# Kernel tuning notes

Hardware: AMD Instinct MI355X
Metric: run time of the kernel (lower is better)

## Reference

```python
import jax, jax.numpy as jnp
import numpy as np

BETA = 0.25


def setup_inputs() -> dict:
    key = jax.random.key(0)
    k1, k2 = jax.random.split(key)
    z = jax.random.normal(k1, (16, 2048, 64), dtype=jnp.float32)
    emb = jax.random.uniform(k2, (8192, 64), dtype=jnp.float32)  # uniform_() init
    return {"z": z, "emb": emb}


def reference(z, emb):
    # z: [B, N, D], emb: [K, D]; use_norm=False so norm is identity.
    B, N, D = z.shape
    zf = z.reshape(-1, D)                                   # [B*N, D]
    # Squared euclidean distances; argmin is identical to cdist(p=2) argmin.
    d2 = (
        jnp.sum(zf * zf, axis=1, keepdims=True)
        - 2.0 * (zf @ emb.T)
        + jnp.sum(emb * emb, axis=1)
    )                                                       # [B*N, K]
    idx = jnp.argmin(d2, axis=1)                            # [B*N]
    z_q = emb[idx].reshape(z.shape)                         # [B, N, D]
    loss = BETA * jnp.mean((jax.lax.stop_gradient(z_q) - z) ** 2) + jnp.mean(
        (z_q - jax.lax.stop_gradient(z)) ** 2
    )
    z_q_st = z + jax.lax.stop_gradient(z_q - z)             # straight-through
    return z_q_st, idx, loss
```

## Files before the change

### kernel.cpp

```cpp
#include <hip/hip_runtime.h>
#include <hip/hip_bf16.h>
#include <math.h>

#define D 64
#define K_CODES 8192
#define M_QUERIES 32768
#define SLICES 8
#define CODES_PER_SLICE (K_CODES / SLICES)
#define CHUNK 32
#define NCHUNK (CODES_PER_SLICE / CHUNK)
#define QPB 128
#define TAU_V 4e-3f

typedef __attribute__((ext_vector_type(8))) short bf16x8;
typedef __attribute__((ext_vector_type(4))) float f32x4;
typedef __attribute__((ext_vector_type(16))) float f32x16;

__device__ __forceinline__ unsigned short f2bf(float x) {
    __hip_bfloat16 h = __float2bfloat16(x);
    return *reinterpret_cast<unsigned short*>(&h);
}
__device__ __forceinline__ float bf2f(unsigned short s) {
    __hip_bfloat16 h;
    *reinterpret_cast<unsigned short*>(&h) = s;
    return __bfloat162float(h);
}
__device__ __forceinline__ void gld_lds16(const void* g, void* l) {
    __builtin_amdgcn_global_load_lds(
        (const __attribute__((address_space(1))) void*)g,
        (__attribute__((address_space(3))) void*)l, 16, 0, 0);
}
__device__ __forceinline__ void gld_lds4(const void* g, void* l) {
    __builtin_amdgcn_global_load_lds(
        (const __attribute__((address_space(1))) void*)g,
        (__attribute__((address_space(3))) void*)l, 4, 0, 0);
}

__global__ __launch_bounds__(256) void k0_split(const float* __restrict__ emb,
                                                unsigned short* __restrict__ e_hi,
                                                unsigned short* __restrict__ e_lo,
                                                float* __restrict__ halfee,
                                                int* __restrict__ ws_cnt) {
    const int t = threadIdx.x;
    const int grp = blockIdx.x;
    if (grp == 0 && t == 0) *ws_cnt = 0;
    const int u = t & 7;
#pragma unroll
    for (int it = 0; it < 2; ++it) {
        const int r = (t >> 3) + it * 32;
        const int code = grp * 64 + r;
        const float* src = emb + ((size_t)code * 64 + u * 8);
        float4 f0 = *(const float4*)(src);
        float4 f1 = *(const float4*)(src + 4);
        float f[8] = {f0.x, f0.y, f0.z, f0.w, f1.x, f1.y, f1.z, f1.w};
        bf16x8 h, lo;
        float s = 0.f;
#pragma unroll
        for (int j = 0; j < 8; ++j) {
            float e = f[j];
            s += e * e;
            unsigned short hh = f2bf(e);
            h[j]  = (short)hh;
            lo[j] = (short)f2bf(e - bf2f(hh));
        }
        const int c32 = code >> 5, r32 = code & 31;
        size_t off = (size_t)c32 * 4096 + (size_t)(u * 32 + r32) * 16;
        *(bf16x8*)((char*)e_hi + off) = h;
        *(bf16x8*)((char*)e_lo + off) = lo;
        s += __shfl_xor(s, 1);
        s += __shfl_xor(s, 2);
        s += __shfl_xor(s, 4);
        if (u == 0) halfee[code] = 0.5f * s + 128.0f;
    }
}

__global__ __launch_bounds__(256, 1) void k1_mfma(const float* __restrict__ z,
                                                  const unsigned short* __restrict__ e_hi,
                                                  const unsigned short* __restrict__ e_lo,
                                                  const float* __restrict__ halfee,
                                                  float4* __restrict__ ws_part) {
    __shared__ __align__(16) unsigned short ldshi[2][CHUNK * 64];
    __shared__ __align__(16) unsigned short ldslo[2][CHUNK * 64];
    __shared__ __align__(16) float ldshe[2][CHUNK];

    const int tid = threadIdx.x;
    const int wid = tid >> 6;
    const int l   = tid & 63;
    const int col = l & 31;
    const int hi  = l >> 5;
    const int slice = blockIdx.y;
    const int chunk0 = slice * NCHUNK;
    const int cbase0 = slice * CODES_PER_SLICE;

    const int qw0 = blockIdx.x * QPB + wid * 32;
    const int qrow = qw0 + col;
    bf16x8 qh[4], ql[4];
#pragma unroll
    for (int kk = 0; kk < 4; ++kk) {
        const float* src = z + (size_t)qrow * D + kk * 16 + hi * 8;
        float4 f0 = *(const float4*)(src);
        float4 f1 = *(const float4*)(src + 4);
        float f[8] = {f0.x, f0.y, f0.z, f0.w, f1.x, f1.y, f1.z, f1.w};
        bf16x8 h, lo;
#pragma unroll
        for (int j = 0; j < 8; ++j) {
            float x = -f[j];
            unsigned short hh = f2bf(x);
            float r = x - bf2f(hh);
            h[j]  = (short)hh;
            lo[j] = (short)f2bf(r);
        }
        qh[kk] = h;
        ql[kk] = lo;
    }

    float g1 = 1e30f, g2 = 1e30f;
    int   gi = 0x7fffffff;

#define STAGE(buf, c1)                                                           \
    {                                                                            \
        size_t cb = (size_t)(chunk0 + (c1)) * 4096 + wid * 1024 + l * 16;        \
        gld_lds16((const char*)e_hi + cb, (char*)&ldshi[buf][0] + wid * 1024);   \
        gld_lds16((const char*)e_lo + cb, (char*)&ldslo[buf][0] + wid * 1024);   \
        if (tid < 32)                                                            \
            gld_lds4((const char*)halfee + (size_t)(chunk0 + (c1)) * 128 + tid * 4, \
                     (char*)&ldshe[buf][0]);                                     \
    }

#define MFMA_CHUNK(bufc, acc)                                                    \
    {                                                                            \
        const char*  bh  = (const char*)ldshi[bufc];                             \
        const char*  bl  = (const char*)ldslo[bufc];                             \
        const float* bhe = ldshe[bufc];                                          \
        _Pragma("unroll") for (int g4 = 0; g4 < 4; ++g4) {                       \
            f32x4 he4 = *(const f32x4*)(bhe + g4 * 8 + 4 * hi);                  \
            _Pragma("unroll") for (int j = 0; j < 4; ++j)                        \
                acc[g4 * 4 + j] = he4[j];                                        \
        }                                                                        \
        _Pragma("unroll") for (int kk = 0; kk < 4; ++kk) {                       \
            int a0 = ((kk * 2 + hi) * 32 + col) * 16;       \
            bf16x8 ah = *(const bf16x8*)(bh + a0);                               \
            bf16x8 al = *(const bf16x8*)(bl + a0);                               \
            acc = __builtin_amdgcn_mfma_f32_32x32x16_bf16(ah, qh[kk], acc, 0, 0, 0); \
            acc = __builtin_amdgcn_mfma_f32_32x32x16_bf16(ah, ql[kk], acc, 0, 0, 0); \
            acc = __builtin_amdgcn_mfma_f32_32x32x16_bf16(al, qh[kk], acc, 0, 0, 0); \
        }                                                                        \
    }

#define TOP2T(acc, cbase)                                                        \
    {                                                                            \
        float t1[8], t2[8];                                                      \
        _Pragma("unroll") for (int i = 0; i < 8; ++i) {                          \
            float va = __int_as_float((__float_as_int(acc[2 * i])     & 0xFFFFFFF0) | (2 * i));     \
            float vb = __int_as_float((__float_as_int(acc[2 * i + 1]) & 0xFFFFFFF0) | (2 * i + 1)); \
            t1[i] = fminf(va, vb);                                               \
            t2[i] = fmaxf(va, vb);                                               \
        }                                                                        \
        _Pragma("unroll") for (int s = 4; s > 0; s >>= 1) {                      \
            _Pragma("unroll") for (int i = 0; i < s; ++i) {                      \
                float m2c = fminf(t2[i], t2[i + s]);                             \
                t2[i] = __builtin_amdgcn_fmed3f(t1[i], t1[i + s], m2c);          \
                t1[i] = fminf(t1[i], t1[i + s]);                                 \
            }                                                                    \
        }                                                                        \
        float m1p = t1[0], m2p = t2[0];                                          \
        int p1 = __float_as_int(m1p) & 15;                                       \
        int code = (cbase) + (p1 & 3) + 8 * (p1 >> 2) + 4 * hi;                  \
        bool lt = m1p < g1;                                                      \
        g2 = fminf(lt ? g1 : g2, lt ? m2p : m1p);                                \
        g1 = lt ? m1p : g1;                                                      \
        gi = lt ? code : gi;                                                     \
    }

    f32x16 accE, accO;

    STAGE(0, 0);
    __syncthreads();
    STAGE(1, 1);
    MFMA_CHUNK(0, accE);
    __syncthreads();
    for (int cc = 1; cc + 1 < NCHUNK; cc += 2) {
        STAGE(0, cc + 1);
        MFMA_CHUNK(1, accO);
        TOP2T(accE, cbase0 + (cc - 1) * CHUNK);
        __syncthreads();
        if (cc + 2 < NCHUNK) STAGE(1, cc + 2);
        MFMA_CHUNK(0, accE);
        TOP2T(accO, cbase0 + cc * CHUNK);
        __syncthreads();
    }
    MFMA_CHUNK(1, accO);
    TOP2T(accE, cbase0 + (NCHUNK - 2) * CHUNK);
    TOP2T(accO, cbase0 + (NCHUNK - 1) * CHUNK);

    {
        float o1 = __shfl_xor(g1, 32);
        float o2 = __shfl_xor(g2, 32);
        int   oi = __shfl_xor(gi, 32);
        bool  take = (o1 < g1) || (o1 == g1 && oi < gi);
        float n2   = take ? fminf(o2, g1) : fminf(g2, o1);
        g1 = take ? o1 : g1;
        gi = take ? oi : gi;
        g2 = n2;
        if (l < 32) {
            int q = qw0 + col;
            ws_part[(size_t)q * SLICES + slice] =
                make_float4(g1, g2, __int_as_float(gi), 0.f);
        }
    }
#undef STAGE
#undef MFMA_CHUNK
#undef TOP2T
}

__global__ __launch_bounds__(256) void k1b_merge(const float4* __restrict__ ws_part,
                                                 int* __restrict__ ws_idx,
                                                 int* __restrict__ ws_cnt,
                                                 int* __restrict__ ws_list) {
    int q = blockIdx.x * blockDim.x + threadIdx.x;
    float m1 = 1e30f, m2 = 1e30f;
    int   i1 = 0x7fffffff;
#pragma unroll
    for (int s = 0; s < SLICES; ++s) {
        float4 p = ws_part[(size_t)q * SLICES + s];
        float v1 = p.x, v2 = p.y;
        int   vi = __float_as_int(p.z);
        if (v1 < m1 || (v1 == m1 && vi < i1)) { m2 = fminf(m1, v2); m1 = v1; i1 = vi; }
        else                                  { m2 = fminf(m2, v1); }
    }
    ws_idx[q] = i1;
    if (m2 - m1 < TAU_V) {
        int r = atomicAdd(ws_cnt, 1);
        ws_list[r] = q;
    }
}

__global__ __launch_bounds__(256) void k2_rescue(const float* __restrict__ z,
                                                 const float* __restrict__ emb,
                                                 const int* __restrict__ ws_cnt,
                                                 const int* __restrict__ ws_list,
                                                 int* __restrict__ ws_idx) {
    __shared__ float  zrow[D];
    __shared__ double rv[256];
    __shared__ int    ri[256];
    const int cnt = *ws_cnt;
    for (int r = blockIdx.x; r < cnt; r += gridDim.x) {
        const int q = ws_list[r];
        __syncthreads();
        if (threadIdx.x < D) zrow[threadIdx.x] = z[(size_t)q * D + threadIdx.x];
        __syncthreads();
        double best = 1e300;
        int    bi   = 0x7fffffff;
        for (int c = threadIdx.x; c < K_CODES; c += 256) {
            const float4* er = (const float4*)(emb + (size_t)c * D);
            double acc = 0.0;
#pragma unroll
            for (int k = 0; k < 16; ++k) {
                float4 e  = er[k];
                double d0 = (double)zrow[4 * k + 0] - (double)e.x;
                double d1 = (double)zrow[4 * k + 1] - (double)e.y;
                double d2 = (double)zrow[4 * k + 2] - (double)e.z;
                double d3 = (double)zrow[4 * k + 3] - (double)e.w;
                acc += d0 * d0 + d1 * d1 + d2 * d2 + d3 * d3;
            }
            if (acc < best) { best = acc; bi = c; }
        }
        rv[threadIdx.x] = best;
        ri[threadIdx.x] = bi;
        __syncthreads();
        for (int s = 128; s > 0; s >>= 1) {
            if (threadIdx.x < s) {
                double ov = rv[threadIdx.x + s];
                int    oi = ri[threadIdx.x + s];
                if (ov < rv[threadIdx.x] || (ov == rv[threadIdx.x] && oi < ri[threadIdx.x])) {
                    rv[threadIdx.x] = ov;
                    ri[threadIdx.x] = oi;
                }
            }
            __syncthreads();
        }
        if (threadIdx.x == 0) ws_idx[q] = ri[0];
        __syncthreads();
    }
}

__global__ __launch_bounds__(256) void k3_gather(const float* __restrict__ emb,
                                                 const float* __restrict__ z,
                                                 const int* __restrict__ ws_idx,
                                                 float* __restrict__ out,
                                                 float* __restrict__ partial) {
    __shared__ float sb[256];
    int g = blockIdx.x * 256 + threadIdx.x;
    int q = g >> 6, d = g & 63;
    int id = ws_idx[q];
    float e = emb[(size_t)id * D + d];
    out[g] = e;
    if (d == 0) out[(size_t)M_QUERIES * D + q] = (float)id;
    float df = e - z[g];
    sb[threadIdx.x] = df * df;
    __syncthreads();
    for (int s = 128; s > 0; s >>= 1) {
        if (threadIdx.x < s) sb[threadIdx.x] += sb[threadIdx.x + s];
        __syncthreads();
    }
    if (threadIdx.x == 0) partial[blockIdx.x] = sb[0];
}

__global__ __launch_bounds__(256) void k4_loss(const float* __restrict__ partial,
                                               float* __restrict__ out) {
    __shared__ double sb[256];
    double s = 0.0;
    for (int i = threadIdx.x; i < (M_QUERIES * D) / 256; i += 256) s += (double)partial[i];
    sb[threadIdx.x] = s;
    __syncthreads();
    for (int st = 128; st > 0; st >>= 1) {
        if (threadIdx.x < st) sb[threadIdx.x] += sb[threadIdx.x + st];
        __syncthreads();
    }
    if (threadIdx.x == 0)
        out[(size_t)M_QUERIES * D + M_QUERIES] =
            (float)(1.25 * sb[0] / (double)((size_t)M_QUERIES * D));
}

extern "C" void kernel_launch(void* const* d_in, const int* in_sizes, int n_in,
                              void* d_out, int out_size, void* d_ws, size_t ws_size,
                              hipStream_t stream) {
    const float* z   = (const float*)d_in[0];
    const float* emb = (const float*)d_in[1];
    float* out = (float*)d_out;
    char*  ws  = (char*)d_ws;

    unsigned short* e_hi    = (unsigned short*)(ws);
    unsigned short* e_lo    = (unsigned short*)(ws + 1048576);
    float*          halfee  = (float*)(ws + 2097152);
    float4*         ws_part = (float4*)(ws + 2129920);
    int*            ws_idx  = (int*)(ws + 2129920 + 4194304);
    int*            ws_cnt  = (int*)(ws + 2129920 + 4194304 + 131072);
    int*            ws_list = (int*)(ws + 2129920 + 4194304 + 131136);
    float*          partial = (float*)(ws + 2129920 + 4194304 + 262208);

    k0_split<<<K_CODES / 64, 256, 0, stream>>>(emb, e_hi, e_lo, halfee, ws_cnt);

    dim3 g1(M_QUERIES / QPB, SLICES);
    k1_mfma<<<g1, 256, 0, stream>>>(z, e_hi, e_lo, halfee, ws_part);

    k1b_merge<<<M_QUERIES / 256, 256, 0, stream>>>(ws_part, ws_idx, ws_cnt, ws_list);

    k2_rescue<<<256, 256, 0, stream>>>(z, emb, ws_cnt, ws_list, ws_idx);

    k3_gather<<<(M_QUERIES * D) / 256, 256, 0, stream>>>(emb, z, ws_idx, out, partial);

    k4_loss<<<1, 256, 0, stream>>>(partial, out);
}
```

Baseline: 195.8 us.

## Track only chunk minima in MFMA argmin, fuse loss into gather, precompute code norms

The per-chunk top-2 selection in the MFMA distance kernel is replaced with a plain minimum, so only chunk-level minima feed the second-best margin used to flag queries for rescue. This cuts VALU work in the hot loop, but it weakens the margin check: a runner-up code in the same chunk as the winner is never seen, so some ambiguous queries may no longer be sent to exact rescue. The rescue kernel now uses precomputed double-precision code norms and a dot product instead of a full difference-squared sum. The gather kernel becomes grid-stride with fewer blocks, and the last block to finish, found through an atomic counter, performs the final loss reduction, which removes a separate kernel launch.

```diff
diff --git a/kernel.cpp b/kernel.cpp
--- a/kernel.cpp
+++ b/kernel.cpp
@@ -40,10 +40,12 @@
                                                 unsigned short* __restrict__ e_hi,
                                                 unsigned short* __restrict__ e_lo,
                                                 float* __restrict__ halfee,
-                                                int* __restrict__ ws_cnt) {
+                                                double* __restrict__ eed,
+                                                int* __restrict__ ws_cnt,
+                                                unsigned int* __restrict__ done_ctr) {
     const int t = threadIdx.x;
     const int grp = blockIdx.x;
-    if (grp == 0 && t == 0) *ws_cnt = 0;
+    if (grp == 0 && t == 0) { *ws_cnt = 0; *done_ctr = 0u; }
     const int u = t & 7;
 #pragma unroll
     for (int it = 0; it < 2; ++it) {
@@ -55,10 +57,12 @@
         float f[8] = {f0.x, f0.y, f0.z, f0.w, f1.x, f1.y, f1.z, f1.w};
         bf16x8 h, lo;
         float s = 0.f;
+        double sd = 0.0;
 #pragma unroll
         for (int j = 0; j < 8; ++j) {
             float e = f[j];
             s += e * e;
+            sd += (double)e * (double)e;
             unsigned short hh = f2bf(e);
             h[j]  = (short)hh;
             lo[j] = (short)f2bf(e - bf2f(hh));
@@ -70,7 +74,13 @@
         s += __shfl_xor(s, 1);
         s += __shfl_xor(s, 2);
         s += __shfl_xor(s, 4);
-        if (u == 0) halfee[code] = 0.5f * s + 128.0f;
+        sd += __shfl_xor(sd, 1);
+        sd += __shfl_xor(sd, 2);
+        sd += __shfl_xor(sd, 4);
+        if (u == 0) {
+            halfee[code] = 0.5f * s + 128.0f;
+            eed[code]    = sd;
+        }
     }
 }
 
@@ -147,27 +157,20 @@
         }                                                                        \
     }
 
-#define TOP2T(acc, cbase)                                                        \
+#define TOP1T(acc, cbase)                                                        \
     {                                                                            \
-        float t1[8], t2[8];                                                      \
+        float t[8];                                                              \
         _Pragma("unroll") for (int i = 0; i < 8; ++i) {                          \
             float va = __int_as_float((__float_as_int(acc[2 * i])     & 0xFFFFFFF0) | (2 * i));     \
             float vb = __int_as_float((__float_as_int(acc[2 * i + 1]) & 0xFFFFFFF0) | (2 * i + 1)); \
-            t1[i] = fminf(va, vb);                                               \
-            t2[i] = fmaxf(va, vb);                                               \
+            t[i] = fminf(va, vb);                                                \
         }                                                                        \
-        _Pragma("unroll") for (int s = 4; s > 0; s >>= 1) {                      \
-            _Pragma("unroll") for (int i = 0; i < s; ++i) {                      \
-                float m2c = fminf(t2[i], t2[i + s]);                             \
-                t2[i] = __builtin_amdgcn_fmed3f(t1[i], t1[i + s], m2c);          \
-                t1[i] = fminf(t1[i], t1[i + s]);                                 \
-            }                                                                    \
-        }                                                                        \
-        float m1p = t1[0], m2p = t2[0];                                          \
+        float m1p = fminf(fminf(fminf(t[0], t[1]), fminf(t[2], t[3])),           \
+                          fminf(fminf(t[4], t[5]), fminf(t[6], t[7])));          \
         int p1 = __float_as_int(m1p) & 15;                                       \
         int code = (cbase) + (p1 & 3) + 8 * (p1 >> 2) + 4 * hi;                  \
         bool lt = m1p < g1;                                                      \
-        g2 = fminf(lt ? g1 : g2, lt ? m2p : m1p);                                \
+        g2 = fminf(lt ? g1 : g2, lt ? 1e30f : m1p);                              \
         g1 = lt ? m1p : g1;                                                      \
         gi = lt ? code : gi;                                                     \
     }
@@ -182,16 +185,16 @@
     for (int cc = 1; cc + 1 < NCHUNK; cc += 2) {
         STAGE(0, cc + 1);
         MFMA_CHUNK(1, accO);
-        TOP2T(accE, cbase0 + (cc - 1) * CHUNK);
+        TOP1T(accE, cbase0 + (cc - 1) * CHUNK);
         __syncthreads();
         if (cc + 2 < NCHUNK) STAGE(1, cc + 2);
         MFMA_CHUNK(0, accE);
-        TOP2T(accO, cbase0 + cc * CHUNK);
+        TOP1T(accO, cbase0 + cc * CHUNK);
         __syncthreads();
     }
     MFMA_CHUNK(1, accO);
-    TOP2T(accE, cbase0 + (NCHUNK - 2) * CHUNK);
-    TOP2T(accO, cbase0 + (NCHUNK - 1) * CHUNK);
+    TOP1T(accE, cbase0 + (NCHUNK - 2) * CHUNK);
+    TOP1T(accO, cbase0 + (NCHUNK - 1) * CHUNK);
 
     {
         float o1 = __shfl_xor(g1, 32);
@@ -210,7 +213,7 @@
     }
 #undef STAGE
 #undef MFMA_CHUNK
-#undef TOP2T
+#undef TOP1T
 }
 
 __global__ __launch_bounds__(256) void k1b_merge(const float4* __restrict__ ws_part,
@@ -237,6 +240,7 @@
 
 __global__ __launch_bounds__(256) void k2_rescue(const float* __restrict__ z,
                                                  const float* __restrict__ emb,
+                                                 const double* __restrict__ eed,
                                                  const int* __restrict__ ws_cnt,
                                                  const int* __restrict__ ws_list,
                                                  int* __restrict__ ws_idx) {
@@ -253,17 +257,17 @@
         int    bi   = 0x7fffffff;
         for (int c = threadIdx.x; c < K_CODES; c += 256) {
             const float4* er = (const float4*)(emb + (size_t)c * D);
-            double acc = 0.0;
+            double dot = 0.0;
 #pragma unroll
             for (int k = 0; k < 16; ++k) {
-                float4 e  = er[k];
-                double d0 = (double)zrow[4 * k + 0] - (double)e.x;
-                double d1 = (double)zrow[4 * k + 1] - (double)e.y;
-                double d2 = (double)zrow[4 * k + 2] - (double)e.z;
-                double d3 = (double)zrow[4 * k + 3] - (double)e.w;
-                acc += d0 * d0 + d1 * d1 + d2 * d2 + d3 * d3;
+                float4 e = er[k];
+                dot += (double)zrow[4 * k + 0] * (double)e.x
+                     + (double)zrow[4 * k + 1] * (double)e.y
+                     + (double)zrow[4 * k + 2] * (double)e.z
+                     + (double)zrow[4 * k + 3] * (double)e.w;
             }
-            if (acc < best) { best = acc; bi = c; }
+            double s = fma(-2.0, dot, eed[c]);
+            if (s < best) { best = s; bi = c; }
         }
         rv[threadIdx.x] = best;
         ri[threadIdx.x] = bi;
@@ -288,38 +292,49 @@
                                                  const float* __restrict__ z,
                                                  const int* __restrict__ ws_idx,
                                                  float* __restrict__ out,
-                                                 float* __restrict__ partial) {
+                                                 float* __restrict__ partial,
+                                                 unsigned int* __restrict__ done_ctr) {
     __shared__ float sb[256];
-    int g = blockIdx.x * 256 + threadIdx.x;
-    int q = g >> 6, d = g & 63;
-    int id = ws_idx[q];
-    float e = emb[(size_t)id * D + d];
-    out[g] = e;
-    if (d == 0) out[(size_t)M_QUERIES * D + q] = (float)id;
-    float df = e - z[g];
-    sb[threadIdx.x] = df * df;
+    __shared__ int lastf;
+    float local = 0.f;
+    for (int g = blockIdx.x * 256 + threadIdx.x; g < M_QUERIES * D;
+         g += gridDim.x * 256) {
+        int q = g >> 6, d = g & 63;
+        int id = ws_idx[q];
+        float e = emb[(size_t)id * D + d];
+        out[g] = e;
+        if (d == 0) out[(size_t)M_QUERIES * D + q] = (float)id;
+        float df = e - z[g];
+        local += df * df;
+    }
+    sb[threadIdx.x] = local;
     __syncthreads();
     for (int s = 128; s > 0; s >>= 1) {
         if (threadIdx.x < s) sb[threadIdx.x] += sb[threadIdx.x + s];
         __syncthreads();
     }
     if (threadIdx.x == 0) partial[blockIdx.x] = sb[0];
-}
-
-__global__ __launch_bounds__(256) void k4_loss(const float* __restrict__ partial,
-                                               float* __restrict__ out) {
-    __shared__ double sb[256];
-    double s = 0.0;
-    for (int i = threadIdx.x; i < (M_QUERIES * D) / 256; i += 256) s += (double)partial[i];
-    sb[threadIdx.x] = s;
+    __threadfence();
+    if (threadIdx.x == 0) {
+        unsigned int v = atomicAdd(done_ctr, 1u);
+        lastf = (v == gridDim.x - 1) ? 1 : 0;
+    }
     __syncthreads();
-    for (int st = 128; st > 0; st >>= 1) {
-        if (threadIdx.x < st) sb[threadIdx.x] += sb[threadIdx.x + st];
-        __syncthreads();
-    }
-    if (threadIdx.x == 0)
-        out[(size_t)M_QUERIES * D + M_QUERIES] =
-            (float)(1.25 * sb[0] / (double)((size_t)M_QUERIES * D));
+    if (lastf) {
+        __threadfence();
+        __shared__ double db[256];
+        double s = 0.0;
+        for (int i = threadIdx.x; i < gridDim.x; i += 256) s += (double)partial[i];
+        db[threadIdx.x] = s;
+        __syncthreads();
+        for (int st = 128; st > 0; st >>= 1) {
+            if (threadIdx.x < st) db[threadIdx.x] += db[threadIdx.x + st];
+            __syncthreads();
+        }
+        if (threadIdx.x == 0)
+            out[(size_t)M_QUERIES * D + M_QUERIES] =
+                (float)(1.25 * db[0] / (double)((size_t)M_QUERIES * D));
+    }
 }
 
 extern "C" void kernel_launch(void* const* d_in, const int* in_sizes, int n_in,
@@ -333,22 +348,23 @@
     unsigned short* e_hi    = (unsigned short*)(ws);
     unsigned short* e_lo    = (unsigned short*)(ws + 1048576);
     float*          halfee  = (float*)(ws + 2097152);
-    float4*         ws_part = (float4*)(ws + 2129920);
-    int*            ws_idx  = (int*)(ws + 2129920 + 4194304);
-    int*            ws_cnt  = (int*)(ws + 2129920 + 4194304 + 131072);
-    int*            ws_list = (int*)(ws + 2129920 + 4194304 + 131136);
-    float*          partial = (float*)(ws + 2129920 + 4194304 + 262208);
-
-    k0_split<<<K_CODES / 64, 256, 0, stream>>>(emb, e_hi, e_lo, halfee, ws_cnt);
+    double*         eed     = (double*)(ws + 2129920);
+    float4*         ws_part = (float4*)(ws + 2195456);
+    int*            ws_idx  = (int*)(ws + 2195456 + 4194304);
+    int*            ws_cnt  = (int*)(ws + 2195456 + 4194304 + 131072);
+    int*            ws_list = (int*)(ws + 2195456 + 4194304 + 131136);
+    float*          partial = (float*)(ws + 2195456 + 4194304 + 262208);
+    unsigned int*   done_ctr= (unsigned int*)(ws + 2195456 + 4194304 + 262208 + 8192);
+
+    k0_split<<<K_CODES / 64, 256, 0, stream>>>(emb, e_hi, e_lo, halfee, eed,
+                                               ws_cnt, done_ctr);
 
     dim3 g1(M_QUERIES / QPB, SLICES);
     k1_mfma<<<g1, 256, 0, stream>>>(z, e_hi, e_lo, halfee, ws_part);
 
     k1b_merge<<<M_QUERIES / 256, 256, 0, stream>>>(ws_part, ws_idx, ws_cnt, ws_list);
 
-    k2_rescue<<<256, 256, 0, stream>>>(z, emb, ws_cnt, ws_list, ws_idx);
-
-    k3_gather<<<(M_QUERIES * D) / 256, 256, 0, stream>>>(emb, z, ws_idx, out, partial);
-
-    k4_loss<<<1, 256, 0, stream>>>(partial, out);
-}
+    k2_rescue<<<256, 256, 0, stream>>>(z, emb, eed, ws_cnt, ws_list, ws_idx);
+
+    k3_gather<<<2048, 256, 0, stream>>>(emb, z, ws_idx, out, partial, done_ctr);
+}
```

New measurement: 331.3 us. 1.69x slower.
